# Optimization experiments

Measured on AMD Instinct MI355X. Metric: run time of the kernel, lower is better.

Reference implementation:

```python
import jax, jax.numpy as jnp
import numpy as np

N_NODES = 100000
N_EDGES = 200000
N_GRAPHS = 4096
NODE_DIM = 256
OUT_DIM = 768
LAYERS = 4
NODE_FEATS = 9
EDGE_FEATS = 3
NODE_VOCAB = 119  # max categorical size across node features (padded)
EDGE_VOCAB = 22   # max categorical size across edge features (padded)


def setup_inputs() -> dict:
    key = jax.random.key(0)
    ks = jax.random.split(key, 16)
    x_cat = jax.random.randint(ks[0], (N_NODES, NODE_FEATS), 0, 2)
    edge_attr = jax.random.randint(ks[1], (N_EDGES, EDGE_FEATS), 0, 2)
    edge_index = jax.random.randint(ks[2], (2, N_EDGES), 0, N_NODES)
    batch = jnp.sort(jax.random.randint(ks[3], (N_NODES,), 0, N_GRAPHS))
    s = 0.02
    node_emb = jax.random.normal(ks[4], (NODE_FEATS, NODE_VOCAB, NODE_DIM), jnp.float32) * s
    edge_emb = jax.random.normal(ks[5], (EDGE_FEATS, EDGE_VOCAB, NODE_DIM), jnp.float32) * s
    W1 = jax.random.normal(ks[6], (LAYERS, NODE_DIM, 2 * NODE_DIM), jnp.float32) * s
    b1 = jnp.zeros((LAYERS, 2 * NODE_DIM), jnp.float32)
    W2 = jax.random.normal(ks[7], (LAYERS, 2 * NODE_DIM, NODE_DIM), jnp.float32) * s
    b2 = jnp.zeros((LAYERS, NODE_DIM), jnp.float32)
    pW1 = jax.random.normal(ks[8], (NODE_DIM, NODE_DIM), jnp.float32) * s
    pb1 = jnp.zeros((NODE_DIM,), jnp.float32)
    pW2 = jax.random.normal(ks[9], (NODE_DIM, OUT_DIM), jnp.float32) * s
    pb2 = jnp.zeros((OUT_DIM,), jnp.float32)
    return {
        "x_cat": x_cat, "edge_attr": edge_attr, "edge_index": edge_index, "batch": batch,
        "node_emb": node_emb, "edge_emb": edge_emb,
        "W1": W1, "b1": b1, "W2": W2, "b2": b2,
        "pW1": pW1, "pb1": pb1, "pW2": pW2, "pb2": pb2,
    }


def _encode(tables, idx):
    # tables: [F, V, D], idx: [N, F] -> sum over features of embedding lookups -> [N, D]
    return jnp.sum(jax.vmap(lambda tbl, i: tbl[i], in_axes=(0, 1))(tables, idx), axis=0)


def reference(x_cat, edge_attr, edge_index, batch, node_emb, edge_emb,
              W1, b1, W2, b2, pW1, pb1, pW2, pb2):
    x = _encode(node_emb, x_cat)          # [N, D]
    e = _encode(edge_emb, edge_attr)      # [E, D]
    src, dst = edge_index[0], edge_index[1]
    for l in range(LAYERS):
        # GINEConv: aggr = sum_{j in N(i)} relu(x_j + e_ij); out = mlp((1+eps)*x_i + aggr), eps=0
        msg = jax.nn.relu(x[src] + e)                                  # [E, D]
        agg = jax.ops.segment_sum(msg, dst, num_segments=N_NODES)     # [N, D]
        h = x + agg
        h = jax.nn.relu(h @ W1[l] + b1[l]) @ W2[l] + b2[l]
        x = jax.nn.relu(h)
    g = jax.ops.segment_sum(x, batch, num_segments=N_GRAPHS)          # [G, D]
    g = jax.nn.relu(g @ pW1 + pb1) @ pW2 + pb2                         # [G, OUT]
    norm = jnp.maximum(jnp.linalg.norm(g, axis=-1, keepdims=True), 1e-12)
    return g / norm
```

## Files before the change

kernel.cpp:

```cpp
#include <hip/hip_runtime.h>

#define N_NODES 100000
#define N_NODES_PAD 100032
#define N_EDGES 200000
#define N_GRAPHS 4096
#define D 256
#define D2 512
#define OUTD 768
#define LAYERS 4
#define NODE_FEATS 9
#define EDGE_FEATS 3
#define NODE_VOCAB 119
#define EDGE_VOCAB 22
#define BM 64
#define GB 8

typedef __attribute__((ext_vector_type(8))) short bf16x8;
typedef __attribute__((ext_vector_type(4))) float f32x4;
typedef unsigned short ushort_t;
typedef unsigned int uint_t;

__device__ __forceinline__ ushort_t f2b(float f) {
    union { float f; uint_t u; } x; x.f = f;
    uint_t r = (x.u + 0x7FFFu + ((x.u >> 16) & 1u)) >> 16;
    return (ushort_t)r;
}
__device__ __forceinline__ float b2f(ushort_t u) {
    union { uint_t u; float f; } x; x.u = ((uint_t)u) << 16;
    return x.f;
}

__device__ __forceinline__ int lower_bound_i(const int* a, int n, int v) {
    int lo = 0, hi = n;
    while (lo < hi) { int mid = (lo + hi) >> 1; if (a[mid] < v) lo = mid + 1; else hi = mid; }
    return lo;
}

__global__ __launch_bounds__(256) void encode_nodes_k(const int* __restrict__ xcat,
                                                      const float* __restrict__ tab,
                                                      ushort_t* __restrict__ X) {
    int n = blockIdx.x, d = threadIdx.x;
    float acc = 0.f;
#pragma unroll
    for (int f = 0; f < NODE_FEATS; ++f) {
        int idx = xcat[n * NODE_FEATS + f];
        acc += tab[((size_t)f * NODE_VOCAB + idx) * D + d];
    }
    X[(size_t)n * D + d] = f2b(acc);
}

__global__ __launch_bounds__(256) void count_k(const int* __restrict__ eidx, int* deg) {
    int e = blockIdx.x * 256 + threadIdx.x;
    if (e < N_EDGES) atomicAdd(&deg[eidx[N_EDGES + e]], 1);
}

#define SCAN_B 1024
__global__ __launch_bounds__(256) void scan1_k(const int* __restrict__ deg,
                                               int* __restrict__ excl, int* __restrict__ bsum) {
    __shared__ int sh[256];
    int b = blockIdx.x, t = threadIdx.x;
    int base = b * SCAN_B + t * 4;
    int d0 = (base + 0) < N_NODES ? deg[base + 0] : 0;
    int d1 = (base + 1) < N_NODES ? deg[base + 1] : 0;
    int d2 = (base + 2) < N_NODES ? deg[base + 2] : 0;
    int d3 = (base + 3) < N_NODES ? deg[base + 3] : 0;
    int s = d0 + d1 + d2 + d3;
    sh[t] = s; __syncthreads();
    for (int off = 1; off < 256; off <<= 1) {
        int x = (t >= off) ? sh[t - off] : 0;
        __syncthreads();
        sh[t] += x;
        __syncthreads();
    }
    int incl = sh[t];
    int ex = incl - s;
    if (base + 0 < N_NODES) excl[base + 0] = ex;
    if (base + 1 < N_NODES) excl[base + 1] = ex + d0;
    if (base + 2 < N_NODES) excl[base + 2] = ex + d0 + d1;
    if (base + 3 < N_NODES) excl[base + 3] = ex + d0 + d1 + d2;
    if (t == 255) bsum[b] = incl;
}

__global__ void scan2_k(int* bsum, int nb) {
    __shared__ int sh[128];
    int t = threadIdx.x;
    int v = (t < nb) ? bsum[t] : 0;
    sh[t] = v; __syncthreads();
    for (int off = 1; off < 128; off <<= 1) {
        int x = (t >= off) ? sh[t - off] : 0;
        __syncthreads();
        sh[t] += x;
        __syncthreads();
    }
    if (t < nb) bsum[t] = sh[t] - v;
}

__global__ __launch_bounds__(256) void scan3_k(int* __restrict__ offs, int* __restrict__ cursor,
                                               const int* __restrict__ bsum) {
    int i = blockIdx.x * 256 + threadIdx.x;
    if (i < N_NODES) {
        int v = offs[i] + bsum[i >> 10];
        offs[i] = v;
        cursor[i] = v;
    }
}

__global__ __launch_bounds__(256) void fill_k(const int* __restrict__ eidx,
                                              const int* __restrict__ eattr,
                                              int* cursor, int2* __restrict__ elist) {
    int e = blockIdx.x * 256 + threadIdx.x;
    if (e < N_EDGES) {
        int src = eidx[e];
        int dst = eidx[N_EDGES + e];
        int pa = eattr[e * EDGE_FEATS + 0] | (eattr[e * EDGE_FEATS + 1] << 8)
               | (eattr[e * EDGE_FEATS + 2] << 16);
        int pos = atomicAdd(&cursor[dst], 1);
        elist[pos] = make_int2(src, pa);
    }
}

__global__ __launch_bounds__(256) void gather_k(const ushort4* __restrict__ X4,
                                                const float4* __restrict__ eemb4,
                                                const int* __restrict__ offs,
                                                const int* __restrict__ deg,
                                                const int2* __restrict__ elist,
                                                ushort4* __restrict__ H4) {
    int n = blockIdx.x * 4 + (threadIdx.x >> 6);
    int lane = threadIdx.x & 63;
    int start = offs[n], dg = deg[n];
    ushort4 xv = X4[(size_t)n * 64 + lane];
    float acc[4] = {b2f(xv.x), b2f(xv.y), b2f(xv.z), b2f(xv.w)};
    for (int i = 0; i < dg; i += 2) {
        bool has1 = (i + 1 < dg);
        int2 s0 = elist[start + i];
        int2 s1 = has1 ? elist[start + i + 1] : s0;
        ushort4 v0 = X4[(size_t)s0.x * 64 + lane];
        ushort4 v1 = X4[(size_t)s1.x * 64 + lane];
        float4 a0 = eemb4[(size_t)((s0.y      ) & 255) * 64 + lane];
        float4 a1 = eemb4[((size_t)EDGE_VOCAB + ((s0.y >> 8) & 255)) * 64 + lane];
        float4 a2 = eemb4[((size_t)2 * EDGE_VOCAB + ((s0.y >> 16) & 255)) * 64 + lane];
        acc[0] += fmaxf(b2f(v0.x) + a0.x + a1.x + a2.x, 0.f);
        acc[1] += fmaxf(b2f(v0.y) + a0.y + a1.y + a2.y, 0.f);
        acc[2] += fmaxf(b2f(v0.z) + a0.z + a1.z + a2.z, 0.f);
        acc[3] += fmaxf(b2f(v0.w) + a0.w + a1.w + a2.w, 0.f);
        if (has1) {
            float4 c0 = eemb4[(size_t)((s1.y      ) & 255) * 64 + lane];
            float4 c1 = eemb4[((size_t)EDGE_VOCAB + ((s1.y >> 8) & 255)) * 64 + lane];
            float4 c2 = eemb4[((size_t)2 * EDGE_VOCAB + ((s1.y >> 16) & 255)) * 64 + lane];
            acc[0] += fmaxf(b2f(v1.x) + c0.x + c1.x + c2.x, 0.f);
            acc[1] += fmaxf(b2f(v1.y) + c0.y + c1.y + c2.y, 0.f);
            acc[2] += fmaxf(b2f(v1.z) + c0.z + c1.z + c2.z, 0.f);
            acc[3] += fmaxf(b2f(v1.w) + c0.w + c1.w + c2.w, 0.f);
        }
    }
    ushort4 hv;
    hv.x = f2b(acc[0]); hv.y = f2b(acc[1]); hv.z = f2b(acc[2]); hv.w = f2b(acc[3]);
    H4[(size_t)n * 64 + lane] = hv;
}

__global__ __launch_bounds__(256) void pack1_k(const float* __restrict__ W1, ushort_t* __restrict__ apack) {
    size_t i = (size_t)blockIdx.x * 256 + threadIdx.x;
    int l = (int)(i >> 14);
    int rem = (int)(i & 16383);
    int ntg = rem >> 9;
    int rem2 = rem & 511;
    int kk = rem2 >> 6;
    int lane = rem2 & 63;
    int n = ntg * 16 + (lane & 15);
    int k0 = kk * 32 + (lane >> 4) * 8;
    const float* w = W1 + ((size_t)l * D + k0) * D2 + n;
    ushort_t* o = apack + i * 8;
#pragma unroll
    for (int j = 0; j < 8; ++j) o[j] = f2b(w[(size_t)j * D2]);
}

__global__ __launch_bounds__(256) void pack2_k(const float* __restrict__ W2, ushort_t* __restrict__ bpack) {
    size_t i = (size_t)blockIdx.x * 256 + threadIdx.x;
    int l = (int)(i >> 14);
    int rem = (int)(i & 16383);
    int ntg = rem >> 10;
    int rem2 = rem & 1023;
    int kk = rem2 >> 6;
    int lane = rem2 & 63;
    int n = ntg * 16 + (lane & 15);
    int k0 = kk * 32 + (lane >> 4) * 8;
    const float* w = W2 + ((size_t)l * D2 + k0) * D + n;
    ushort_t* o = bpack + i * 8;
#pragma unroll
    for (int j = 0; j < 8; ++j) o[j] = f2b(w[(size_t)j * D]);
}

#define LDA(h, nt, kk) (*(const bf16x8*)(apack + ((size_t)(((h) * 16 + wid * 2 + (nt)) * 8 + (kk)) * 64 + lane) * 8))
#define LDW(h, nt, kk) (*(const bf16x8*)(bpack + ((size_t)((wid * 2 + (nt)) * 16 + (h) * 8 + (kk)) * 64 + lane) * 8))

__global__ __launch_bounds__(512, 4) void mlp_k(const ushort_t* __restrict__ H,
                                                const ushort_t* __restrict__ apack,
                                                const float* __restrict__ b1,
                                                const ushort_t* __restrict__ bpack,
                                                const float* __restrict__ b2,
                                                ushort_t* __restrict__ X) {
    __shared__ __align__(16) char hA[BM * 512];
    __shared__ __align__(16) char midh[BM * 512];
    const int t = threadIdx.x;
    const int wid = t >> 6, lane = t & 63;
    const int l15 = lane & 15, g = lane >> 4;
    const size_t r0 = (size_t)blockIdx.x * BM;

    {
        const char* src = (const char*)(H + r0 * D);
#pragma unroll
        for (int c = 0; c < 4; ++c) {
            int Lb = (c * 512 + t) * 16;
            int row = Lb >> 9;
            int Sb = Lb ^ ((row & 7) << 4);
            *(uint4*)(hA + Sb) = *(const uint4*)(src + Lb);
        }
    }

    f32x4 acc2[2][4];
#pragma unroll
    for (int a = 0; a < 2; ++a)
#pragma unroll
        for (int b = 0; b < 4; ++b) { f32x4 z = {0.f,0.f,0.f,0.f}; acc2[a][b] = z; }

    bf16x8 a0 = LDA(0, 0, 0), a1 = LDA(0, 1, 0);

    __syncthreads();

#pragma unroll
    for (int half = 0; half < 2; ++half) {
        f32x4 acc1[2][4];
#pragma unroll
        for (int a = 0; a < 2; ++a)
#pragma unroll
            for (int b = 0; b < 4; ++b) { f32x4 z = {0.f,0.f,0.f,0.f}; acc1[a][b] = z; }

#pragma unroll
        for (int kk = 0; kk < 8; ++kk) {
            bf16x8 Bf[4];
#pragma unroll
            for (int mt = 0; mt < 4; ++mt) {
                int m = mt * 16 + l15;
                Bf[mt] = *(const bf16x8*)(hA + ((m * 512 + (kk * 32 + g * 8) * 2) ^ ((m & 7) << 4)));
            }
            bf16x8 n0 = a0, n1 = a1;
            if (kk < 7) { n0 = LDA(half, 0, kk + 1); n1 = LDA(half, 1, kk + 1); }
            __builtin_amdgcn_s_setprio(1);
#pragma unroll
            for (int mt = 0; mt < 4; ++mt)
                acc1[0][mt] = __builtin_amdgcn_mfma_f32_16x16x32_bf16(a0, Bf[mt], acc1[0][mt], 0, 0, 0);
#pragma unroll
            for (int mt = 0; mt < 4; ++mt)
                acc1[1][mt] = __builtin_amdgcn_mfma_f32_16x16x32_bf16(a1, Bf[mt], acc1[1][mt], 0, 0, 0);
            __builtin_amdgcn_s_setprio(0);
            a0 = n0; a1 = n1;
        }

        bf16x8 w0 = LDW(half, 0, 0), w1 = LDW(half, 1, 0);

#pragma unroll
        for (int nt = 0; nt < 2; ++nt) {
            int n0l = (wid * 2 + nt) * 16 + g * 4;
            f32x4 bv = *(const f32x4*)(b1 + half * 256 + n0l);
#pragma unroll
            for (int mt = 0; mt < 4; ++mt) {
                int m = mt * 16 + l15;
                ushort_t us[4];
#pragma unroll
                for (int r = 0; r < 4; ++r)
                    us[r] = f2b(fmaxf(acc1[nt][mt][r] + bv[r], 0.f));
                uint2 pk;
                pk.x = (uint_t)us[0] | ((uint_t)us[1] << 16);
                pk.y = (uint_t)us[2] | ((uint_t)us[3] << 16);
                *(uint2*)(midh + ((m * 512 + n0l * 2) ^ ((m & 7) << 4))) = pk;
            }
        }
        __syncthreads();

#pragma unroll
        for (int kk = 0; kk < 8; ++kk) {
            bf16x8 Mf[4];
#pragma unroll
            for (int mt = 0; mt < 4; ++mt) {
                int m = mt * 16 + l15;
                Mf[mt] = *(const bf16x8*)(midh + ((m * 512 + (kk * 32 + g * 8) * 2) ^ ((m & 7) << 4)));
            }
            bf16x8 n0 = w0, n1 = w1;
            if (kk < 7) { n0 = LDW(half, 0, kk + 1); n1 = LDW(half, 1, kk + 1); }
            __builtin_amdgcn_s_setprio(1);
#pragma unroll
            for (int mt = 0; mt < 4; ++mt)
                acc2[0][mt] = __builtin_amdgcn_mfma_f32_16x16x32_bf16(w0, Mf[mt], acc2[0][mt], 0, 0, 0);
#pragma unroll
            for (int mt = 0; mt < 4; ++mt)
                acc2[1][mt] = __builtin_amdgcn_mfma_f32_16x16x32_bf16(w1, Mf[mt], acc2[1][mt], 0, 0, 0);
            __builtin_amdgcn_s_setprio(0);
            w0 = n0; w1 = n1;
        }

        if (half == 0) { a0 = LDA(1, 0, 0); a1 = LDA(1, 1, 0); }
        __syncthreads();
    }

#pragma unroll
    for (int nt = 0; nt < 2; ++nt) {
        int n0 = (wid * 2 + nt) * 16 + g * 4;
        f32x4 bv = *(const f32x4*)(b2 + n0);
#pragma unroll
        for (int mt = 0; mt < 4; ++mt) {
            int m = mt * 16 + l15;
            ushort_t us[4];
#pragma unroll
            for (int r = 0; r < 4; ++r)
                us[r] = f2b(fmaxf(acc2[nt][mt][r] + bv[r], 0.f));
            uint2 pk;
            pk.x = (uint_t)us[0] | ((uint_t)us[1] << 16);
            pk.y = (uint_t)us[2] | ((uint_t)us[3] << 16);
            *(uint2*)(midh + ((m * 512 + n0 * 2) ^ ((m & 7) << 4))) = pk;
        }
    }
    __syncthreads();
    {
        char* dst = (char*)X + r0 * 512;
#pragma unroll
        for (int j = 0; j < 4; ++j) {
            int Lb = t * 64 + j * 16;
            int row = Lb >> 9;
            int Sb = Lb ^ ((row & 7) << 4);
            *(uint4*)(dst + Lb) = *(const uint4*)(midh + Sb);
        }
    }
}

__global__ __launch_bounds__(256) void final_k(const ushort4* __restrict__ X4,
                                               const int* __restrict__ batch,
                                               const float* __restrict__ pW1,
                                               const float* __restrict__ pb1,
                                               const float* __restrict__ pW2,
                                               const float* __restrict__ pb2,
                                               float* __restrict__ out) {
    __shared__ float gin[GB][D];
    __shared__ float mid[GB][D];
    __shared__ float red[GB][256];
    __shared__ int bnd[GB + 1];
    const int g0 = blockIdx.x * GB, t = threadIdx.x;
    const int wid = t >> 6, lane = t & 63;
    if (t <= GB) bnd[t] = lower_bound_i(batch, N_NODES, g0 + t);
    __syncthreads();

#pragma unroll
    for (int qq = 0; qq < 2; ++qq) {
        int q = wid + qq * 4;
        f32x4 a = {0.f, 0.f, 0.f, 0.f};
        for (int n = bnd[q]; n < bnd[q + 1]; ++n) {
            ushort4 v = X4[(size_t)n * 64 + lane];
            a.x += b2f(v.x); a.y += b2f(v.y); a.z += b2f(v.z); a.w += b2f(v.w);
        }
        *(f32x4*)&gin[q][lane * 4] = a;
    }
    __syncthreads();

    {
        float m_[GB];
        float bb = pb1[t];
#pragma unroll
        for (int q = 0; q < GB; ++q) m_[q] = bb;
        for (int k = 0; k < D; ++k) {
            float w = pW1[(size_t)k * D + t];
#pragma unroll
            for (int q = 0; q < GB; ++q) m_[q] += gin[q][k] * w;
        }
#pragma unroll
        for (int q = 0; q < GB; ++q) mid[q][t] = fmaxf(m_[q], 0.f);
    }
    __syncthreads();

    float a0[GB], a1[GB], a2[GB];
    {
        float b0 = pb2[t], b1_ = pb2[t + 256], b2_ = pb2[t + 512];
#pragma unroll
        for (int q = 0; q < GB; ++q) { a0[q] = b0; a1[q] = b1_; a2[q] = b2_; }
        for (int k = 0; k < D; ++k) {
            float w0 = pW2[(size_t)k * OUTD + t];
            float w1 = pW2[(size_t)k * OUTD + 256 + t];
            float w2 = pW2[(size_t)k * OUTD + 512 + t];
#pragma unroll
            for (int q = 0; q < GB; ++q) {
                float mv = mid[q][k];
                a0[q] += mv * w0; a1[q] += mv * w1; a2[q] += mv * w2;
            }
        }
    }
#pragma unroll
    for (int q = 0; q < GB; ++q)
        red[q][t] = a0[q] * a0[q] + a1[q] * a1[q] + a2[q] * a2[q];
    __syncthreads();
    for (int s = 128; s > 0; s >>= 1) {
        if (t < s) {
#pragma unroll
            for (int q = 0; q < GB; ++q) red[q][t] += red[q][t + s];
        }
        __syncthreads();
    }
#pragma unroll
    for (int q = 0; q < GB; ++q) {
        float inv = 1.f / fmaxf(sqrtf(red[q][0]), 1e-12f);
        out[(size_t)(g0 + q) * OUTD + t]       = a0[q] * inv;
        out[(size_t)(g0 + q) * OUTD + 256 + t] = a1[q] * inv;
        out[(size_t)(g0 + q) * OUTD + 512 + t] = a2[q] * inv;
    }
}

extern "C" void kernel_launch(void* const* d_in, const int* in_sizes, int n_in,
                              void* d_out, int out_size, void* d_ws, size_t ws_size,
                              hipStream_t stream) {
    const int*   x_cat      = (const int*)d_in[0];
    const int*   edge_attr  = (const int*)d_in[1];
    const int*   edge_index = (const int*)d_in[2];
    const int*   batch      = (const int*)d_in[3];
    const float* node_emb   = (const float*)d_in[4];
    const float* edge_emb   = (const float*)d_in[5];
    const float* W1  = (const float*)d_in[6];
    const float* b1  = (const float*)d_in[7];
    const float* W2  = (const float*)d_in[8];
    const float* b2  = (const float*)d_in[9];
    const float* pW1 = (const float*)d_in[10];
    const float* pb1 = (const float*)d_in[11];
    const float* pW2 = (const float*)d_in[12];
    const float* pb2 = (const float*)d_in[13];
    float* out = (float*)d_out;

    char* p = (char*)d_ws;
    auto carve = [&](size_t bytes) { char* q = p; p += (bytes + 255) & ~(size_t)255; return q; };
    ushort_t* X      = (ushort_t*)carve((size_t)N_NODES_PAD * D * 2);
    ushort_t* H      = (ushort_t*)carve((size_t)N_NODES_PAD * D * 2);
    int*      deg    = (int*)carve((size_t)N_NODES * 4);
    int*      offs   = (int*)carve((size_t)(N_NODES + 8) * 4);
    int*      cursor = (int*)carve((size_t)(N_NODES + 8) * 4);
    int*      bsum   = (int*)carve(1024);
    int2*     elist  = (int2*)carve((size_t)N_EDGES * 8);
    ushort_t* apack1 = (ushort_t*)carve((size_t)LAYERS * 32 * 8 * 64 * 8 * 2);
    ushort_t* bpack2 = (ushort_t*)carve((size_t)LAYERS * 16 * 16 * 64 * 8 * 2);

    const int NB = (N_NODES + SCAN_B - 1) / SCAN_B;

    pack1_k<<<256, 256, 0, stream>>>(W1, apack1);
    pack2_k<<<256, 256, 0, stream>>>(W2, bpack2);
    hipMemsetAsync(deg, 0, (size_t)N_NODES * 4, stream);
    count_k<<<(N_EDGES + 255) / 256, 256, 0, stream>>>(edge_index, deg);
    scan1_k<<<NB, 256, 0, stream>>>(deg, offs, bsum);
    scan2_k<<<1, 128, 0, stream>>>(bsum, NB);
    scan3_k<<<(N_NODES + 255) / 256, 256, 0, stream>>>(offs, cursor, bsum);
    fill_k<<<(N_EDGES + 255) / 256, 256, 0, stream>>>(edge_index, edge_attr, cursor, elist);

    encode_nodes_k<<<N_NODES, 256, 0, stream>>>(x_cat, node_emb, X);

    for (int l = 0; l < LAYERS; ++l) {
        gather_k<<<N_NODES / 4, 256, 0, stream>>>((const ushort4*)X, (const float4*)edge_emb,
                                                  offs, deg, elist, (ushort4*)H);
        mlp_k<<<N_NODES_PAD / BM, 512, 0, stream>>>(
            H,
            apack1 + (size_t)l * 32 * 8 * 64 * 8,
            b1 + (size_t)l * D2,
            bpack2 + (size_t)l * 16 * 16 * 64 * 8,
            b2 + (size_t)l * D,
            X);
    }

    final_k<<<N_GRAPHS / GB, 256, 0, stream>>>((const ushort4*)X, batch, pW1, pb1, pW2, pb2, out);
}
```

Baseline: 729.3 us.

## Split MLP hidden dimension into quarters to halve LDS and register use

```diff
diff --git a/kernel.cpp b/kernel.cpp
--- a/kernel.cpp
+++ b/kernel.cpp
@@ -190,8 +190,8 @@
     for (int j = 0; j < 8; ++j) o[j] = f2b(w[(size_t)j * D]);
 }
 
-#define LDA(h, nt, kk) (*(const bf16x8*)(apack + ((size_t)(((h) * 16 + wid * 2 + (nt)) * 8 + (kk)) * 64 + lane) * 8))
-#define LDW(h, nt, kk) (*(const bf16x8*)(bpack + ((size_t)((wid * 2 + (nt)) * 16 + (h) * 8 + (kk)) * 64 + lane) * 8))
+#define LDA1(q, kk) (*(const bf16x8*)(apack + ((size_t)(((q) * 8 + wid) * 8 + (kk)) * 64 + lane) * 8))
+#define LDW2(nt, kkg) (*(const bf16x8*)(bpack + ((size_t)((wid * 2 + (nt)) * 16 + (kkg)) * 64 + lane) * 8))
 
 __global__ __launch_bounds__(512, 4) void mlp_k(const ushort_t* __restrict__ H,
                                                 const ushort_t* __restrict__ apack,
@@ -200,7 +200,7 @@
                                                 const float* __restrict__ b2,
                                                 ushort_t* __restrict__ X) {
     __shared__ __align__(16) char hA[BM * 512];
-    __shared__ __align__(16) char midh[BM * 512];
+    __shared__ __align__(16) char midq[BM * 256];
     const int t = threadIdx.x;
     const int wid = t >> 6, lane = t & 63;
     const int l15 = lane & 15, g = lane >> 4;
@@ -223,17 +223,15 @@
 #pragma unroll
         for (int b = 0; b < 4; ++b) { f32x4 z = {0.f,0.f,0.f,0.f}; acc2[a][b] = z; }
 
-    bf16x8 a0 = LDA(0, 0, 0), a1 = LDA(0, 1, 0);
-
-    __syncthreads();
-
-#pragma unroll
-    for (int half = 0; half < 2; ++half) {
-        f32x4 acc1[2][4];
-#pragma unroll
-        for (int a = 0; a < 2; ++a)
-#pragma unroll
-            for (int b = 0; b < 4; ++b) { f32x4 z = {0.f,0.f,0.f,0.f}; acc1[a][b] = z; }
+    bf16x8 af = LDA1(0, 0);
+
+    __syncthreads();
+
+#pragma unroll
+    for (int q = 0; q < 4; ++q) {
+        f32x4 acc1[4];
+#pragma unroll
+        for (int b = 0; b < 4; ++b) { f32x4 z = {0.f,0.f,0.f,0.f}; acc1[b] = z; }
 
 #pragma unroll
         for (int kk = 0; kk < 8; ++kk) {
@@ -243,50 +241,46 @@
                 int m = mt * 16 + l15;
                 Bf[mt] = *(const bf16x8*)(hA + ((m * 512 + (kk * 32 + g * 8) * 2) ^ ((m & 7) << 4)));
             }
-            bf16x8 n0 = a0, n1 = a1;
-            if (kk < 7) { n0 = LDA(half, 0, kk + 1); n1 = LDA(half, 1, kk + 1); }
+            bf16x8 afn = af;
+            if (kk < 7) afn = LDA1(q, kk + 1);
             __builtin_amdgcn_s_setprio(1);
 #pragma unroll
             for (int mt = 0; mt < 4; ++mt)
-                acc1[0][mt] = __builtin_amdgcn_mfma_f32_16x16x32_bf16(a0, Bf[mt], acc1[0][mt], 0, 0, 0);
-#pragma unroll
-            for (int mt = 0; mt < 4; ++mt)
-                acc1[1][mt] = __builtin_amdgcn_mfma_f32_16x16x32_bf16(a1, Bf[mt], acc1[1][mt], 0, 0, 0);
+                acc1[mt] = __builtin_amdgcn_mfma_f32_16x16x32_bf16(af, Bf[mt], acc1[mt], 0, 0, 0);
             __builtin_amdgcn_s_setprio(0);
-            a0 = n0; a1 = n1;
-        }
-
-        bf16x8 w0 = LDW(half, 0, 0), w1 = LDW(half, 1, 0);
-
-#pragma unroll
-        for (int nt = 0; nt < 2; ++nt) {
-            int n0l = (wid * 2 + nt) * 16 + g * 4;
-            f32x4 bv = *(const f32x4*)(b1 + half * 256 + n0l);
+            af = afn;
+        }
+
+        bf16x8 w0 = LDW2(0, q * 4 + 0), w1 = LDW2(1, q * 4 + 0);
+
+        {
+            int n0l = wid * 16 + g * 4;
+            f32x4 bv = *(const f32x4*)(b1 + q * 128 + n0l);
 #pragma unroll
             for (int mt = 0; mt < 4; ++mt) {
                 int m = mt * 16 + l15;
                 ushort_t us[4];
 #pragma unroll
                 for (int r = 0; r < 4; ++r)
-                    us[r] = f2b(fmaxf(acc1[nt][mt][r] + bv[r], 0.f));
+                    us[r] = f2b(fmaxf(acc1[mt][r] + bv[r], 0.f));
                 uint2 pk;
                 pk.x = (uint_t)us[0] | ((uint_t)us[1] << 16);
                 pk.y = (uint_t)us[2] | ((uint_t)us[3] << 16);
-                *(uint2*)(midh + ((m * 512 + n0l * 2) ^ ((m & 7) << 4))) = pk;
+                *(uint2*)(midq + ((m * 256 + n0l * 2) ^ ((m & 7) << 4))) = pk;
             }
         }
         __syncthreads();
 
 #pragma unroll
-        for (int kk = 0; kk < 8; ++kk) {
+        for (int kk2 = 0; kk2 < 4; ++kk2) {
             bf16x8 Mf[4];
 #pragma unroll
             for (int mt = 0; mt < 4; ++mt) {
                 int m = mt * 16 + l15;
-                Mf[mt] = *(const bf16x8*)(midh + ((m * 512 + (kk * 32 + g * 8) * 2) ^ ((m & 7) << 4)));
+                Mf[mt] = *(const bf16x8*)(midq + ((m * 256 + (kk2 * 32 + g * 8) * 2) ^ ((m & 7) << 4)));
             }
-            bf16x8 n0 = w0, n1 = w1;
-            if (kk < 7) { n0 = LDW(half, 0, kk + 1); n1 = LDW(half, 1, kk + 1); }
+            bf16x8 w0n = w0, w1n = w1;
+            if (kk2 < 3) { w0n = LDW2(0, q * 4 + kk2 + 1); w1n = LDW2(1, q * 4 + kk2 + 1); }
             __builtin_amdgcn_s_setprio(1);
 #pragma unroll
             for (int mt = 0; mt < 4; ++mt)
@@ -295,10 +289,10 @@
             for (int mt = 0; mt < 4; ++mt)
                 acc2[1][mt] = __builtin_amdgcn_mfma_f32_16x16x32_bf16(w1, Mf[mt], acc2[1][mt], 0, 0, 0);
             __builtin_amdgcn_s_setprio(0);
-            w0 = n0; w1 = n1;
-        }
-
-        if (half == 0) { a0 = LDA(1, 0, 0); a1 = LDA(1, 1, 0); }
+            w0 = w0n; w1 = w1n;
+        }
+
+        if (q < 3) af = LDA1(q + 1, 0);
         __syncthreads();
     }
 
@@ -316,7 +310,7 @@
             uint2 pk;
             pk.x = (uint_t)us[0] | ((uint_t)us[1] << 16);
             pk.y = (uint_t)us[2] | ((uint_t)us[3] << 16);
-            *(uint2*)(midh + ((m * 512 + n0 * 2) ^ ((m & 7) << 4))) = pk;
+            *(uint2*)(hA + ((m * 512 + n0 * 2) ^ ((m & 7) << 4))) = pk;
         }
     }
     __syncthreads();
@@ -327,7 +321,7 @@
             int Lb = t * 64 + j * 16;
             int row = Lb >> 9;
             int Sb = Lb ^ ((row & 7) << 4);
-            *(uint4*)(dst + Lb) = *(const uint4*)(midh + Sb);
+            *(uint4*)(dst + Lb) = *(const uint4*)(hA + Sb);
         }
     }
 }
```

After: 767.8 us. +5.3%, slower.
